# Kernel tuning notes

Measured on AMD Instinct MI355X. Metric: run time of the kernel, lower is better.

Reference implementation:

```python
import jax, jax.numpy as jnp
import numpy as np
from jax import lax

D_MODEL = 256
VOCAB = 512
D_INNER = 512          # expand=2
D_STATE = 64
D_CONV = 4
HEADDIM = 32
NHEADS = D_INNER // HEADDIM  # 16
NGROUPS = 1
CHUNK = 64
D_IN_PROJ = 2 * D_INNER + 2 * NGROUPS * D_STATE + NHEADS  # 1168
CONV_DIM = D_INNER + 2 * NGROUPS * D_STATE               # 640


def setup_inputs() -> dict:
    key = jax.random.key(0)
    ks = jax.random.split(key, 8)
    B, L = 8, 4096
    input_ids = jax.random.randint(ks[0], (B, L), 0, VOCAB)
    rn = lambda k, shp, sc: (jax.random.normal(k, shp) * sc).astype(jnp.float32)
    embed_w = rn(ks[1], (VOCAB, D_MODEL), 0.02).at[0].set(0.0)  # padding_idx=0
    in_proj_w = rn(ks[2], (D_IN_PROJ, D_MODEL), D_MODEL ** -0.5)
    conv_w = rn(ks[3], (CONV_DIM, D_CONV), 0.2)
    conv_b = jnp.zeros((CONV_DIM,), jnp.float32)
    A_log = jnp.log(jax.random.uniform(ks[4], (NHEADS,), minval=1.0, maxval=16.0)).astype(jnp.float32)
    D_skip = jnp.ones((NHEADS,), jnp.float32)
    dt0 = jax.random.uniform(ks[5], (NHEADS,), minval=1e-3, maxval=0.1)
    dt_bias = jnp.log(jnp.expm1(dt0)).astype(jnp.float32)  # inverse softplus
    gate_norm_w = jnp.ones((D_INNER,), jnp.float32)
    out_proj_w = rn(ks[6], (D_MODEL, D_INNER), D_INNER ** -0.5)
    norm_w = jnp.ones((D_MODEL,), jnp.float32)
    return dict(input_ids=input_ids, embed_w=embed_w, in_proj_w=in_proj_w,
                conv_w=conv_w, conv_b=conv_b, A_log=A_log, D_skip=D_skip,
                dt_bias=dt_bias, gate_norm_w=gate_norm_w, out_proj_w=out_proj_w,
                norm_w=norm_w)


def _rmsnorm(x, w, eps):
    return x * lax.rsqrt(jnp.mean(x * x, axis=-1, keepdims=True) + eps) * w


def _segsum(a):
    # a: (..., T) -> (..., T, T); out[q,s] = sum_{s+1..q} a, -inf above diag
    T = a.shape[-1]
    c = jnp.cumsum(a, axis=-1)
    seg = c[..., :, None] - c[..., None, :]
    mask = jnp.tril(jnp.ones((T, T), bool))
    return jnp.where(mask, seg, -jnp.inf)


def _ssd(X, A, Bm, Cm):
    # X:(b,l,h,p) already *dt ; A:(b,l,h)=dt*A_head ; Bm,Cm:(b,l,n)
    b, l, h, p = X.shape
    n = Bm.shape[-1]
    c, q = l // CHUNK, CHUNK
    X = X.reshape(b, c, q, h, p)
    A = A.reshape(b, c, q, h).transpose(0, 3, 1, 2)        # (b,h,c,q)
    Bm = Bm.reshape(b, c, q, n)
    Cm = Cm.reshape(b, c, q, n)
    A_cs = jnp.cumsum(A, axis=-1)                           # (b,h,c,q)
    Lmat = jnp.exp(_segsum(A))                              # (b,h,c,q,q)
    # intra-chunk (diagonal block) output
    Y_diag = jnp.einsum('bcqn,bckn,bhcqk,bckhp->bcqhp', Cm, Bm, Lmat, X)
    # states carried to end of each chunk
    decay_states = jnp.exp(A_cs[..., -1:] - A_cs)           # (b,h,c,q)
    states = jnp.einsum('bckn,bhck,bckhp->bchpn', Bm, decay_states, X)
    chunk_decay = jnp.exp(A_cs[..., -1])                    # (b,h,c)
    def step(hprev, inp):
        dec, st = inp
        return dec[..., None, None] * hprev + st, hprev
    _, prev = lax.scan(step, jnp.zeros((b, h, p, n), X.dtype),
                       (chunk_decay.transpose(2, 0, 1), states.transpose(1, 0, 2, 3, 4)))
    prev = prev.transpose(1, 0, 2, 3, 4)                    # (b,c,h,p,n)
    Y_off = jnp.einsum('bcqn,bchpn,bhcq->bcqhp', Cm, prev, jnp.exp(A_cs))
    return (Y_diag + Y_off).reshape(b, l, h, p)


def _mamba2(u, in_proj_w, conv_w, conv_b, A_log, D_skip, dt_bias, gate_norm_w, out_proj_w):
    B, L, _ = u.shape
    zxbcdt = u @ in_proj_w.T                                # (B,L,1168)
    z = zxbcdt[..., :D_INNER]
    xBC = zxbcdt[..., D_INNER:D_INNER + CONV_DIM]
    dt = zxbcdt[..., D_INNER + CONV_DIM:]                   # (B,L,H)
    # causal depthwise conv + silu
    xBC = lax.conv_general_dilated(xBC.transpose(0, 2, 1), conv_w[:, None, :],
                                   (1,), [(D_CONV - 1, 0)],
                                   dimension_numbers=('NCH', 'OIH', 'NCH'),
                                   feature_group_count=CONV_DIM)
    xBC = jax.nn.silu(xBC + conv_b[None, :, None]).transpose(0, 2, 1)
    x = xBC[..., :D_INNER].reshape(B, L, NHEADS, HEADDIM)
    Bm = xBC[..., D_INNER:D_INNER + D_STATE]
    Cm = xBC[..., D_INNER + D_STATE:]
    dt = jax.nn.softplus(dt + dt_bias)                      # (B,L,H)
    A = -jnp.exp(A_log)                                     # (H,)
    y = _ssd(x * dt[..., None], dt * A, Bm, Cm)
    y = y + D_skip[None, None, :, None] * x
    y = y.reshape(B, L, D_INNER)
    y = _rmsnorm(y * jax.nn.silu(z), gate_norm_w, 1e-5)     # RMSNormGated
    return y @ out_proj_w.T


def reference(input_ids, embed_w, in_proj_w, conv_w, conv_b, A_log, D_skip,
              dt_bias, gate_norm_w, out_proj_w, norm_w):
    x = embed_w[input_ids]                                  # (B,L,D)
    u = _rmsnorm(x, norm_w, 1e-6)
    x = x + _mamba2(u, in_proj_w, conv_w, conv_b, A_log, D_skip,
                    dt_bias, gate_norm_w, out_proj_w)
    logits = x @ embed_w.T                                  # tied lm_head
    return logits
```

## Files before the change

### kernel.cpp

```cpp
#include <hip/hip_runtime.h>
#include <cstdint>
#include <cstddef>

#define TOK    32768
#define BATCH  8
#define SEQ    4096
#define DMODEL 256
#define DINNER 512
#define DSTATE 64
#define NH     16
#define HD     32
#define DPROJ  1168
#define NPAD   1280
#define CONVD  640
#define VOCAB  512
#define HGRP   4
#define TS     132

typedef __attribute__((ext_vector_type(8))) short bf16x8;
typedef __attribute__((ext_vector_type(4))) float f32x4;

__device__ __forceinline__ unsigned short f2bf(float f) {
    unsigned u = __float_as_uint(f);
    u += 0x7fffu + ((u >> 16) & 1u);
    return (unsigned short)(u >> 16);
}
__device__ __forceinline__ float bf2f(short s) {
    return __uint_as_float(((unsigned)(unsigned short)s) << 16);
}
__device__ __forceinline__ unsigned cvtpk(float lo, float hi) {
    unsigned r;
    asm("v_cvt_pk_bf16_f32 %0, %1, %2" : "=v"(r) : "v"(lo), "v"(hi));
    return r;
}
__device__ __forceinline__ float fsilu(float s) {
    return s * __builtin_amdgcn_rcpf(1.f + __expf(-s));
}
__device__ __forceinline__ float sp(float v) {
    return v > 20.f ? v : __logf(1.f + __expf(v));
}

__device__ __forceinline__ void gload16(const short* src, short* dst) {
    __builtin_amdgcn_global_load_lds((const __attribute__((address_space(1))) void*)src,
                                     (__attribute__((address_space(3))) void*)dst, 16, 0, 0);
}

#define U16_OFF   0
#define Z16_OFF   (U16_OFF  + (size_t)TOK*128)
#define XBC_OFF   (Z16_OFF  + (size_t)TOK*256)
#define DTS_OFF   (XBC_OFF  + (size_t)TOK*320)
#define ACS_OFF   (DTS_OFF  + (size_t)TOK*16)
#define CDEC_OFF  (ACS_OFF  + (size_t)BATCH*NH*64*64)
#define WP_OFF    (CDEC_OFF + (size_t)BATCH*NH*64)
#define WO_OFF    (WP_OFF   + 163840)
#define WE_OFF    (WO_OFF   + 65536)
#define UNION_OFF (WE_OFF   + 65536)
#define UNION_FL  ((size_t)BATCH*64*NH*2048)
#define Y16_SUB   ((size_t)TOK*256)
#define WS_FLOATS (UNION_OFF + UNION_FL)

__global__ void k_diag(float* out, float wsmb) {
    if (blockIdx.x == 0 && threadIdx.x == 0) out[0] = wsmb;
}

__global__ void k_cvt(const float* __restrict__ s, short* __restrict__ d, int nsrc, int ntot) {
    int i = blockIdx.x * 256 + threadIdx.x;
    if (i < ntot) d[i] = (i < nsrc) ? (short)f2bf(s[i]) : (short)0;
}
__global__ void k_cvt_gate(const float* __restrict__ s, const float* __restrict__ gw,
                           short* __restrict__ d, int ntot) {
    int i = blockIdx.x * 256 + threadIdx.x;
    if (i < ntot) d[i] = (short)f2bf(s[i] * gw[i & (DINNER - 1)]);
}

__global__ void k_embed(const int* __restrict__ ids, const float* __restrict__ embed,
                        const float* __restrict__ norm_w, short* __restrict__ u16) {
    int t = blockIdx.x;
    int lane = threadIdx.x;
    int id = ids[t];
    float4 v = ((const float4*)(embed + (size_t)id * DMODEL))[lane];
    float ss = v.x*v.x + v.y*v.y + v.z*v.z + v.w*v.w;
    #pragma unroll
    for (int o = 32; o > 0; o >>= 1) ss += __shfl_down(ss, o);
    ss = __shfl(ss, 0);
    float r = rsqrtf(ss * (1.0f / DMODEL) + 1e-6f);
    float4 w = ((const float4*)norm_w)[lane];
    unsigned p0 = cvtpk(v.x * r * w.x, v.y * r * w.y);
    unsigned p1 = cvtpk(v.z * r * w.z, v.w * r * w.w);
    ((uint2*)(u16 + (size_t)t * DMODEL))[lane] = make_uint2(p0, p1);
}

template<int MODE>
__global__ __launch_bounds__(512) void k_gemm_mfma(
    const short* __restrict__ A, const short* __restrict__ B, int K,
    float* __restrict__ outF, short* __restrict__ z16, short* __restrict__ xbc,
    float* __restrict__ dts, const float* __restrict__ dt_bias,
    const float* __restrict__ cw, const float* __restrict__ cb) {
    __shared__ __align__(16) short SM[32768];
    constexpr int NX = (MODE == 0) ? (NPAD / 128) : (VOCAB / 128);
    int tid = threadIdx.x;
    int bid = blockIdx.x;
    int slot = bid >> 3;
    int m0 = (((bid & 7) * 32) + slot / NX) << 7;
    int n0 = (slot % NX) << 7;
    int wave = tid >> 6, lane = tid & 63;
    int wm = wave >> 1, wn = wave & 1;
    int lr = lane & 15, lg = lane >> 4;
    const f32x4 zer = {0.f, 0.f, 0.f, 0.f};
    f32x4 acc[2][4];
    #pragma unroll
    for (int i = 0; i < 2; i++)
        #pragma unroll
        for (int j = 0; j < 4; j++) acc[i][j] = zer;

    const bool isXBC = (MODE == 0) && (n0 >= 512) && (n0 < 1152);
    const bool atStart = (m0 & (SEQ - 1)) == 0;
    const bool haloLane = isXBC && (wm == 0) && !atStart && (lr < 3);
    f32x4 hacc[4];
    #pragma unroll
    for (int j = 0; j < 4; j++) hacc[j] = zer;
    const bf16x8 hz = {0, 0, 0, 0, 0, 0, 0, 0};
    bf16x8 hc0 = hz, hc1 = hz, hn0 = hz, hn1 = hz;

    const int nK = K >> 6;
    const int slo = lane >> 3;
    const int skb = ((lane & 7) ^ slo) << 3;

    {
        #pragma unroll
        for (int j = 0; j < 2; j++) {
            int row = wave * 16 + j * 8 + slo;
            gload16(A + (size_t)(m0 + row) * K + skb, SM + (wave * 2 + j) * 512);
            gload16(B + (size_t)(n0 + row) * K + skb, SM + 16384 + (wave * 2 + j) * 512);
        }
        if (haloLane) {
            hc0 = *(const bf16x8*)(A + (size_t)(m0 - 3 + lr) * K + lg * 8);
            hc1 = *(const bf16x8*)(A + (size_t)(m0 - 3 + lr) * K + 32 + lg * 8);
        }
    }
    __syncthreads();

    for (int kt = 0; kt < nK; ++kt) {
        if (kt + 1 < nK) {
            int k0 = (kt + 1) << 6;
            int nb = ((kt + 1) & 1) * 8192;
            #pragma unroll
            for (int j = 0; j < 2; j++) {
                int row = wave * 16 + j * 8 + slo;
                gload16(A + (size_t)(m0 + row) * K + k0 + skb, SM + nb + (wave * 2 + j) * 512);
                gload16(B + (size_t)(n0 + row) * K + k0 + skb, SM + 16384 + nb + (wave * 2 + j) * 512);
            }
            if (haloLane) {
                hn0 = *(const bf16x8*)(A + (size_t)(m0 - 3 + lr) * K + k0 + lg * 8);
                hn1 = *(const bf16x8*)(A + (size_t)(m0 - 3 + lr) * K + k0 + 32 + lg * 8);
            }
        }
        const short* CA = SM + (kt & 1) * 8192;
        const short* CB = SM + 16384 + (kt & 1) * 8192;
        #pragma unroll
        for (int kk = 0; kk < 2; kk++) {
            int sw = (((kk << 2) + lg) ^ (lr & 7)) << 3;
            bf16x8 af[2], bfr[4];
            #pragma unroll
            for (int mi = 0; mi < 2; mi++)
                af[mi] = *(const bf16x8*)&CA[(wm * 32 + mi * 16 + lr) * 64 + sw];
            #pragma unroll
            for (int ni = 0; ni < 4; ni++)
                bfr[ni] = *(const bf16x8*)&CB[(wn * 64 + ni * 16 + lr) * 64 + sw];
            #pragma unroll
            for (int mi = 0; mi < 2; mi++)
                #pragma unroll
                for (int ni = 0; ni < 4; ni++)
                    acc[mi][ni] = __builtin_amdgcn_mfma_f32_16x16x32_bf16(af[mi], bfr[ni], acc[mi][ni], 0, 0, 0);
            if (isXBC && wm == 0) {
                bf16x8 h = (kk == 0) ? hc0 : hc1;
                #pragma unroll
                for (int ni = 0; ni < 4; ni++)
                    hacc[ni] = __builtin_amdgcn_mfma_f32_16x16x32_bf16(h, bfr[ni], hacc[ni], 0, 0, 0);
            }
        }
        __syncthreads();
        hc0 = hn0; hc1 = hn1;
    }

    if (isXBC) {
        short* Tile = SM;
        #pragma unroll
        for (int mi = 0; mi < 2; mi++)
            #pragma unroll
            for (int ni = 0; ni < 4; ni++)
                #pragma unroll
                for (int r = 0; r < 4; r++) {
                    int row = wm * 32 + mi * 16 + lg * 4 + r;
                    int col = wn * 64 + ni * 16 + lr;
                    float v = acc[mi][ni][r];
                    float vo = __shfl_xor(v, 1);
                    if (!(lr & 1))
                        *(unsigned*)&Tile[(3 + row) * TS + col] = cvtpk(v, vo);
                }
        if (wm == 0 && lg == 0) {
            #pragma unroll
            for (int ni = 0; ni < 4; ni++)
                #pragma unroll
                for (int r = 0; r < 3; r++)
                    Tile[r * TS + wn * 64 + ni * 16 + lr] = (short)f2bf(hacc[ni][r]);
        }
        __syncthreads();
        int cp = tid & 63, rg = tid >> 6;
        int colb = cp * 2;
        int ch = (n0 - 512) + colb;
        float c0w0 = cw[ch * 4], c0w1 = cw[ch * 4 + 1], c0w2 = cw[ch * 4 + 2], c0w3 = cw[ch * 4 + 3];
        float c1w0 = cw[ch * 4 + 4], c1w1 = cw[ch * 4 + 5], c1w2 = cw[ch * 4 + 6], c1w3 = cw[ch * 4 + 7];
        float b0v = cb[ch], b1v = cb[ch + 1];
        int rbase = rg * 16;
        unsigned w0 = *(const unsigned*)&Tile[(rbase + 0) * TS + colb];
        unsigned w1 = *(const unsigned*)&Tile[(rbase + 1) * TS + colb];
        unsigned w2 = *(const unsigned*)&Tile[(rbase + 2) * TS + colb];
        for (int i = 0; i < 16; i++) {
            unsigned w3 = *(const unsigned*)&Tile[(rbase + i + 3) * TS + colb];
            float s0 = b0v, s1 = b1v;
            s0 = fmaf(bf2f((short)(w0 & 0xffffu)), c0w0, s0); s1 = fmaf(bf2f((short)(w0 >> 16)), c1w0, s1);
            s0 = fmaf(bf2f((short)(w1 & 0xffffu)), c0w1, s0); s1 = fmaf(bf2f((short)(w1 >> 16)), c1w1, s1);
            s0 = fmaf(bf2f((short)(w2 & 0xffffu)), c0w2, s0); s1 = fmaf(bf2f((short)(w2 >> 16)), c1w2, s1);
            s0 = fmaf(bf2f((short)(w3 & 0xffffu)), c0w3, s0); s1 = fmaf(bf2f((short)(w3 >> 16)), c1w3, s1);
            s0 = fsilu(s0);
            s1 = fsilu(s1);
            *(unsigned*)&xbc[(size_t)(m0 + rbase + i) * CONVD + ch] = cvtpk(s0, s1);
            w0 = w1; w1 = w2; w2 = w3;
        }
        return;
    }

    #pragma unroll
    for (int mi = 0; mi < 2; mi++) {
        #pragma unroll
        for (int r = 0; r < 4; r++) {
            int row = m0 + wm * 32 + mi * 16 + lg * 4 + r;
            #pragma unroll
            for (int ni = 0; ni < 4; ni++) {
                int col = n0 + wn * 64 + ni * 16 + lr;
                float v = acc[mi][ni][r];
                if (MODE == 0) {
                    if (n0 < 512) {
                        float vo = __shfl_xor(v, 1);
                        if (!(lr & 1))
                            *(unsigned*)&z16[(size_t)row * DINNER + col] = cvtpk(v, vo);
                    } else if (wn == 0 && ni == 0) {
                        dts[(size_t)row * NH + lr] = sp(v + dt_bias[lr]);
                    }
                } else {
                    outF[(size_t)row * VOCAB + col] = v;
                }
            }
        }
    }
}

__global__ __launch_bounds__(512) void k_outproj(
    const short* __restrict__ Y16, const short* __restrict__ z16,
    const short* __restrict__ Wo, const int* __restrict__ ids,
    const float* __restrict__ embed, short* __restrict__ xf16) {
    __shared__ __align__(16) short As[8192];
    __shared__ __align__(16) short Bs[8192];
    __shared__ float rmsS[128];
    int tid = threadIdx.x;
    int bid = blockIdx.x;
    int slot = bid >> 3;
    int m0 = (((bid & 7) * 32) + (slot >> 1)) << 7;
    int n0 = (slot & 1) << 7;
    int wave = tid >> 6, lane = tid & 63;
    int wm = wave >> 1, wn = wave & 1;
    int lr = lane & 15, lg = lane >> 4;
    const f32x4 zer = {0.f, 0.f, 0.f, 0.f};
    f32x4 acc[2][4];
    #pragma unroll
    for (int i = 0; i < 2; i++)
        #pragma unroll
        for (int j = 0; j < 4; j++) acc[i][j] = zer;

    const int arow = tid >> 2;
    const int ac0 = (tid & 3) * 2;
    const int slo = lane >> 3;
    const int skb = ((lane & 7) ^ slo) << 3;
    float ssq = 0.f;

    for (int kt = 0; kt < 8; ++kt) {
        int k0 = kt << 6;
        #pragma unroll
        for (int j = 0; j < 2; j++) {
            int row = wave * 16 + j * 8 + slo;
            gload16(Wo + (size_t)(n0 + row) * DINNER + k0 + skb, Bs + (wave * 2 + j) * 512);
        }
        union { int4 v; short s[8]; } y0u, y1u, z0u, z1u;
        const size_t rbase = (size_t)(m0 + arow) * DINNER + k0 + ac0 * 8;
        y0u.v = *(const int4*)(Y16 + rbase);
        y1u.v = *(const int4*)(Y16 + rbase + 8);
        z0u.v = *(const int4*)(z16 + rbase);
        z1u.v = *(const int4*)(z16 + rbase + 8);
        unsigned pk[8];
        #pragma unroll
        for (int e = 0; e < 4; e++) {
            float g0 = bf2f(y0u.s[2*e])     * fsilu(bf2f(z0u.s[2*e]));
            float g1 = bf2f(y0u.s[2*e + 1]) * fsilu(bf2f(z0u.s[2*e + 1]));
            ssq += g0 * g0 + g1 * g1;
            pk[e] = cvtpk(g0, g1);
        }
        #pragma unroll
        for (int e = 0; e < 4; e++) {
            float g0 = bf2f(y1u.s[2*e])     * fsilu(bf2f(z1u.s[2*e]));
            float g1 = bf2f(y1u.s[2*e + 1]) * fsilu(bf2f(z1u.s[2*e + 1]));
            ssq += g0 * g0 + g1 * g1;
            pk[4 + e] = cvtpk(g0, g1);
        }
        *(int4*)&As[arow * 64 + ((ac0 ^ (arow & 7)) << 3)] = *(int4*)&pk[0];
        *(int4*)&As[arow * 64 + (((ac0 + 1) ^ (arow & 7)) << 3)] = *(int4*)&pk[4];
        __syncthreads();
        #pragma unroll
        for (int kk = 0; kk < 2; kk++) {
            int sw = (((kk << 2) + lg) ^ (lr & 7)) << 3;
            bf16x8 af[2], bfr[4];
            #pragma unroll
            for (int mi = 0; mi < 2; mi++)
                af[mi] = *(const bf16x8*)&As[(wm * 32 + mi * 16 + lr) * 64 + sw];
            #pragma unroll
            for (int ni = 0; ni < 4; ni++)
                bfr[ni] = *(const bf16x8*)&Bs[(wn * 64 + ni * 16 + lr) * 64 + sw];
            #pragma unroll
            for (int mi = 0; mi < 2; mi++)
                #pragma unroll
                for (int ni = 0; ni < 4; ni++)
                    acc[mi][ni] = __builtin_amdgcn_mfma_f32_16x16x32_bf16(af[mi], bfr[ni], acc[mi][ni], 0, 0, 0);
        }
        __syncthreads();
    }
    ssq += __shfl_xor(ssq, 1);
    ssq += __shfl_xor(ssq, 2);
    if ((tid & 3) == 0) rmsS[arow] = rsqrtf(ssq * (1.0f / DINNER) + 1e-5f);
    __syncthreads();

    #pragma unroll
    for (int mi = 0; mi < 2; mi++) {
        #pragma unroll
        for (int r = 0; r < 4; r++) {
            int rl = wm * 32 + mi * 16 + lg * 4 + r;
            int row = m0 + rl;
            int id = ids[row];
            float rm = rmsS[rl];
            #pragma unroll
            for (int ni = 0; ni < 4; ni++) {
                int col = n0 + wn * 64 + ni * 16 + lr;
                float v = acc[mi][ni][r] * rm;
                float vo = __shfl_xor(v, 1);
                if (!(lr & 1)) {
                    float2 res = *(const float2*)&embed[(size_t)id * DMODEL + col];
                    *(unsigned*)&xf16[(size_t)row * DMODEL + col] = cvtpk(v + res.x, vo + res.y);
                }
            }
        }
    }
}

__global__ __launch_bounds__(256) void k_states(const short* __restrict__ xbc, const float* __restrict__ dts,
                                                const float* __restrict__ A_log,
                                                short* __restrict__ st16,
                                                float* __restrict__ acs_g, float* __restrict__ cdec) {
    __shared__ short BsB[64 * 72];
    __shared__ short BT[64 * 72];
    __shared__ short XdS[32 * 72];
    __shared__ __align__(16) short XKP[64 * 32];
    __shared__ float dkS[HGRP][64];
    __shared__ float dtS[64];
    int tid = threadIdx.x;
    int bid = blockIdx.x;
    int hg = bid & 3;
    int bc = bid >> 2;
    int b = bc >> 6, c = bc & 63;
    int h0 = hg * HGRP;
    size_t tbase = (size_t)b * SEQ + (size_t)c * 64;
    int wave = tid >> 6, lane = tid & 63;
    int lr = lane & 15, lg = lane >> 4;

    for (int i = tid; i < 64 * 64; i += 256) {
        int q = i >> 6, n = i & 63;
        BsB[q * 72 + n] = xbc[(tbase + q) * CONVD + DINNER + n];
    }
    {
        int h = h0 + wave;
        float Ah = -__expf(A_log[h]);
        float v = dts[(tbase + lane) * NH + h] * Ah;
        #pragma unroll
        for (int off = 1; off < 64; off <<= 1) {
            float o = __shfl_up(v, off);
            if (lane >= off) v += o;
        }
        acs_g[(((size_t)(b * NH + h)) * 64 + c) * 64 + lane] = v;
        float alast = __shfl(v, 63);
        dkS[wave][lane] = __expf(alast - v);
        if (lane == 0) cdec[(b * NH + h) * 64 + c] = __expf(alast);
    }
    __syncthreads();
    for (int i = tid; i < 64 * 64; i += 256) {
        int k = i >> 6, n = i & 63;
        BT[n * 72 + k] = BsB[k * 72 + n];
    }

    for (int hh = 0; hh < HGRP; hh++) {
        int h = h0 + hh;
        {
            int s = wave * 64 + lane;
            gload16(xbc + (tbase + (s >> 2)) * CONVD + h * HD + (s & 3) * 8, XKP + wave * 512);
        }
        if (tid < 64) dtS[tid] = dts[(tbase + tid) * NH + h];
        __syncthreads();
        for (int i = tid; i < 2048; i += 256) {
            int p = i & 31, k = i >> 5;
            XdS[p * 72 + k] = (short)f2bf(bf2f(XKP[k * 32 + p]) * dtS[k] * dkS[hh][k]);
        }
        __syncthreads();
        {
            int ptile = wave & 1;
            bf16x8 a0 = *(const bf16x8*)&XdS[(ptile * 16 + lr) * 72 + lg * 8];
            bf16x8 a1 = *(const bf16x8*)&XdS[(ptile * 16 + lr) * 72 + 32 + lg * 8];
            size_t base = ((size_t)bc * NH + h) * 2048;
            #pragma unroll
            for (int j = 0; j < 2; j++) {
                int nt = (wave >> 1) * 2 + j;
                bf16x8 b0 = *(const bf16x8*)&BT[(nt * 16 + lr) * 72 + lg * 8];
                bf16x8 b1 = *(const bf16x8*)&BT[(nt * 16 + lr) * 72 + 32 + lg * 8];
                f32x4 z = {0.f, 0.f, 0.f, 0.f};
                z = __builtin_amdgcn_mfma_f32_16x16x32_bf16(a0, b0, z, 0, 0, 0);
                z = __builtin_amdgcn_mfma_f32_16x16x32_bf16(a1, b1, z, 0, 0, 0);
                #pragma unroll
                for (int r = 0; r < 4; r++) {
                    int p = ptile * 16 + lg * 4 + r;
                    float v = z[r];
                    float vo = __shfl_xor(v, 1);
                    if (!(lr & 1)) {
                        int chunk = (nt << 1) | (lr >> 3);
                        *(unsigned*)&st16[base + p * 64 + ((chunk ^ (p & 7)) << 3) + (lr & 7)] = cvtpk(v, vo);
                    }
                }
            }
        }
        __syncthreads();
    }
}

__global__ __launch_bounds__(256) void k_scan(unsigned* __restrict__ st32, const float* __restrict__ cdec) {
    int bid = blockIdx.x;
    int bh = bid >> 2, seg = bid & 3;
    int b = bh >> 4, h = bh & 15;
    int off = seg * 256 + threadIdx.x;
    float p0 = 0.f, p1 = 0.f;
    for (int c = 0; c < 64; c++) {
        float dec = cdec[bh * 64 + c];
        size_t idx = ((((size_t)b * 64 + c) * NH) + h) * 1024 + off;
        unsigned v = st32[idx];
        float s0 = bf2f((short)(v & 0xffffu));
        float s1 = bf2f((short)(v >> 16));
        st32[idx] = cvtpk(p0, p1);
        p0 = fmaf(dec, p0, s0);
        p1 = fmaf(dec, p1, s1);
    }
}

__global__ __launch_bounds__(256) void k_y(const short* __restrict__ xbc, const float* __restrict__ dts,
                                           const short* __restrict__ st16, const float* __restrict__ acs_g,
                                           const float* __restrict__ D_skip, short* __restrict__ Y16) {
    __shared__ short CsB[64 * 72];
    __shared__ short Wsh[64 * 72];
    __shared__ short XtS[32 * 72];
    __shared__ __align__(16) short PtL[32 * 64];
    __shared__ __align__(16) short XKP[64 * 32];
    __shared__ float acsH[64];
    __shared__ float dtS[64];
    int tid = threadIdx.x;
    int bid = blockIdx.x;
    int hg = bid & 3;
    int bc = bid >> 2;
    int b = bc >> 6, c = bc & 63;
    int h0 = hg * HGRP;
    size_t tbase = (size_t)b * SEQ + (size_t)c * 64;
    int wave = tid >> 6, lane = tid & 63;
    int lr = lane & 15, lg = lane >> 4;

    for (int i = tid; i < 64 * 64; i += 256) {
        int q = i >> 6, n = i & 63;
        const short* rowp = xbc + (tbase + q) * CONVD + DINNER;
        Wsh[q * 72 + n] = rowp[n];
        CsB[q * 72 + n] = rowp[DSTATE + n];
    }
    __syncthreads();

    f32x4 macc[4];
    bf16x8 ca0 = *(const bf16x8*)&CsB[(wave * 16 + lr) * 72 + lg * 8];
    bf16x8 ca1 = *(const bf16x8*)&CsB[(wave * 16 + lr) * 72 + 32 + lg * 8];
    {
        #pragma unroll
        for (int ct = 0; ct < 4; ct++) {
            bf16x8 b0 = *(const bf16x8*)&Wsh[(ct * 16 + lr) * 72 + lg * 8];
            bf16x8 b1 = *(const bf16x8*)&Wsh[(ct * 16 + lr) * 72 + 32 + lg * 8];
            f32x4 z = {0.f, 0.f, 0.f, 0.f};
            z = __builtin_amdgcn_mfma_f32_16x16x32_bf16(ca0, b0, z, 0, 0, 0);
            z = __builtin_amdgcn_mfma_f32_16x16x32_bf16(ca1, b1, z, 0, 0, 0);
            macc[ct] = z;
        }
    }
    __syncthreads();

    for (int hh = 0; hh < HGRP; hh++) {
        int h = h0 + hh;
        {
            int s = wave * 64 + lane;
            gload16(xbc + (tbase + (s >> 2)) * CONVD + h * HD + (s & 3) * 8, XKP + wave * 512);
            gload16(st16 + ((size_t)bc * NH + h) * 2048 + s * 8, PtL + wave * 512);
        }
        if (tid < 64) {
            acsH[tid] = acs_g[(((size_t)(b * NH + h)) * 64 + c) * 64 + tid];
            dtS[tid] = dts[(tbase + tid) * NH + h];
        }
        __syncthreads();
        #pragma unroll
        for (int ct = 0; ct < 4; ct++) {
            int k = ct * 16 + lr;
            #pragma unroll
            for (int r = 0; r < 4; r++) {
                int q = wave * 16 + lg * 4 + r;
                float wv = 0.f;
                if (k <= q) wv = macc[ct][r] * __expf(acsH[q] - acsH[k]);
                float wo = __shfl_xor(wv, 1);
                if (!(lr & 1))
                    *(unsigned*)&Wsh[q * 72 + k] = cvtpk(wv, wo);
            }
        }
        for (int i = tid; i < 2048; i += 256) {
            int p = i & 31, k = i >> 5;
            XtS[p * 72 + k] = (short)f2bf(bf2f(XKP[k * 32 + p]) * dtS[k]);
        }
        __syncthreads();
        float eq[4];
        #pragma unroll
        for (int r = 0; r < 4; r++) eq[r] = __expf(acsH[wave * 16 + lg * 4 + r]);
        float dsk = D_skip[h];
        bf16x8 wa0 = *(const bf16x8*)&Wsh[(wave * 16 + lr) * 72 + lg * 8];
        bf16x8 wa1 = *(const bf16x8*)&Wsh[(wave * 16 + lr) * 72 + 32 + lg * 8];
        #pragma unroll
        for (int pt = 0; pt < 2; pt++) {
            int p = pt * 16 + lr;
            bf16x8 xb0 = *(const bf16x8*)&XtS[p * 72 + lg * 8];
            bf16x8 xb1 = *(const bf16x8*)&XtS[p * 72 + 32 + lg * 8];
            f32x4 zd = {0.f, 0.f, 0.f, 0.f};
            zd = __builtin_amdgcn_mfma_f32_16x16x32_bf16(wa0, xb0, zd, 0, 0, 0);
            zd = __builtin_amdgcn_mfma_f32_16x16x32_bf16(wa1, xb1, zd, 0, 0, 0);
            bf16x8 pb0 = *(const bf16x8*)&PtL[p * 64 + ((lg ^ (p & 7)) << 3)];
            bf16x8 pb1 = *(const bf16x8*)&PtL[p * 64 + (((lg + 4) ^ (p & 7)) << 3)];
            f32x4 zo = {0.f, 0.f, 0.f, 0.f};
            zo = __builtin_amdgcn_mfma_f32_16x16x32_bf16(ca0, pb0, zo, 0, 0, 0);
            zo = __builtin_amdgcn_mfma_f32_16x16x32_bf16(ca1, pb1, zo, 0, 0, 0);
            #pragma unroll
            for (int r = 0; r < 4; r++) {
                int q = wave * 16 + lg * 4 + r;
                float xv = bf2f(XKP[q * 32 + p]);
                float v = zd[r] + eq[r] * zo[r] + dsk * xv;
                float vo = __shfl_xor(v, 1);
                if (!(lr & 1))
                    *(unsigned*)&Y16[((tbase + q) * NH + h) * HD + p] = cvtpk(v, vo);
            }
        }
        __syncthreads();
    }
}

extern "C" void kernel_launch(void* const* d_in, const int* in_sizes, int n_in,
                              void* d_out, int out_size, void* d_ws, size_t ws_size,
                              hipStream_t stream) {
    const int*   ids        = (const int*)d_in[0];
    const float* embed_w    = (const float*)d_in[1];
    const float* in_proj_w  = (const float*)d_in[2];
    const float* conv_w     = (const float*)d_in[3];
    const float* conv_b     = (const float*)d_in[4];
    const float* A_log      = (const float*)d_in[5];
    const float* D_skip     = (const float*)d_in[6];
    const float* dt_bias    = (const float*)d_in[7];
    const float* gate_w     = (const float*)d_in[8];
    const float* out_proj_w = (const float*)d_in[9];
    const float* norm_w     = (const float*)d_in[10];
    float* out = (float*)d_out;

    if (ws_size < WS_FLOATS * sizeof(float)) {
        k_diag<<<1, 64, 0, stream>>>(out, (float)(ws_size >> 20));
        return;
    }

    float* ws   = (float*)d_ws;
    short* u16  = (short*)(ws + U16_OFF);
    short* z16  = (short*)(ws + Z16_OFF);
    short* xbc  = (short*)(ws + XBC_OFF);
    float* dts  = ws + DTS_OFF;
    float* acs  = ws + ACS_OFF;
    float* cdec = ws + CDEC_OFF;
    short* Wp   = (short*)(ws + WP_OFF);
    short* Wo   = (short*)(ws + WO_OFF);
    short* We   = (short*)(ws + WE_OFF);
    short* st16 = (short*)(ws + UNION_OFF);
    short* Y16  = (short*)(ws + UNION_OFF + Y16_SUB);
    short* xf16 = (short*)(ws + UNION_OFF);

    k_cvt<<<(NPAD * DMODEL + 255) / 256, 256, 0, stream>>>(in_proj_w, Wp, DPROJ * DMODEL, NPAD * DMODEL);
    k_cvt_gate<<<(DMODEL * DINNER + 255) / 256, 256, 0, stream>>>(out_proj_w, gate_w, Wo, DMODEL * DINNER);
    k_cvt<<<(VOCAB * DMODEL + 255) / 256, 256, 0, stream>>>(embed_w, We, VOCAB * DMODEL, VOCAB * DMODEL);
    k_embed<<<TOK, 64, 0, stream>>>(ids, embed_w, norm_w, u16);
    k_gemm_mfma<0><<<(NPAD / 128) * 256, 512, 0, stream>>>(
        u16, Wp, DMODEL, nullptr, z16, xbc, dts, dt_bias, conv_w, conv_b);
    k_states<<<BATCH * 64 * 4, 256, 0, stream>>>(xbc, dts, A_log, st16, acs, cdec);
    k_scan<<<BATCH * NH * 4, 256, 0, stream>>>((unsigned*)st16, cdec);
    k_y<<<BATCH * 64 * 4, 256, 0, stream>>>(xbc, dts, st16, acs, D_skip, Y16);
    k_outproj<<<(DMODEL / 128) * 256, 512, 0, stream>>>(Y16, z16, Wo, ids, embed_w, xf16);
    k_gemm_mfma<2><<<(VOCAB / 128) * 256, 512, 0, stream>>>(
        xf16, We, DMODEL, out, nullptr, nullptr, nullptr, nullptr, nullptr, nullptr);
}
```

Before: 220.4 us.

## Deepen GEMM prefetch to two stages with explicit vmcnt waits

```diff
diff --git a/kernel.cpp b/kernel.cpp
--- a/kernel.cpp
+++ b/kernel.cpp
@@ -116,45 +116,49 @@
     const bool isXBC = (MODE == 0) && (n0 >= 512) && (n0 < 1152);
     const bool atStart = (m0 & (SEQ - 1)) == 0;
     const bool haloLane = isXBC && (wm == 0) && !atStart && (lr < 3);
+    const bool haloWave = isXBC && (wm == 0) && !atStart;
     f32x4 hacc[4];
     #pragma unroll
     for (int j = 0; j < 4; j++) hacc[j] = zer;
     const bf16x8 hz = {0, 0, 0, 0, 0, 0, 0, 0};
-    bf16x8 hc0 = hz, hc1 = hz, hn0 = hz, hn1 = hz;
+    bf16x8 hA0 = hz, hA1 = hz;
+    bf16x8 hB0 = hz, hB1 = hz;
 
     const int nK = K >> 6;
     const int slo = lane >> 3;
     const int skb = ((lane & 7) ^ slo) << 3;
 
-    {
+    auto stage = [&](int kt2) {
+        int k0 = kt2 << 6;
+        int bsel = (kt2 & 1) * 8192;
         #pragma unroll
         for (int j = 0; j < 2; j++) {
             int row = wave * 16 + j * 8 + slo;
-            gload16(A + (size_t)(m0 + row) * K + skb, SM + (wave * 2 + j) * 512);
-            gload16(B + (size_t)(n0 + row) * K + skb, SM + 16384 + (wave * 2 + j) * 512);
-        }
-        if (haloLane) {
-            hc0 = *(const bf16x8*)(A + (size_t)(m0 - 3 + lr) * K + lg * 8);
-            hc1 = *(const bf16x8*)(A + (size_t)(m0 - 3 + lr) * K + 32 + lg * 8);
-        }
-    }
-    __syncthreads();
-
-    for (int kt = 0; kt < nK; ++kt) {
+            gload16(A + (size_t)(m0 + row) * K + k0 + skb, SM + bsel + (wave * 2 + j) * 512);
+            gload16(B + (size_t)(n0 + row) * K + k0 + skb, SM + 16384 + bsel + (wave * 2 + j) * 512);
+        }
+    };
+
+    stage(0);
+    if (haloLane) {
+        hA0 = *(const bf16x8*)(A + (size_t)(m0 - 3 + lr) * K + lg * 8);
+        hA1 = *(const bf16x8*)(A + (size_t)(m0 - 3 + lr) * K + 32 + lg * 8);
+    }
+    stage(1);
+    if (haloLane) {
+        hB0 = *(const bf16x8*)(A + (size_t)(m0 - 3 + lr) * K + 64 + lg * 8);
+        hB1 = *(const bf16x8*)(A + (size_t)(m0 - 3 + lr) * K + 96 + lg * 8);
+    }
+
+    auto body = [&](int kt, bf16x8& h0, bf16x8& h1) {
         if (kt + 1 < nK) {
-            int k0 = (kt + 1) << 6;
-            int nb = ((kt + 1) & 1) * 8192;
-            #pragma unroll
-            for (int j = 0; j < 2; j++) {
-                int row = wave * 16 + j * 8 + slo;
-                gload16(A + (size_t)(m0 + row) * K + k0 + skb, SM + nb + (wave * 2 + j) * 512);
-                gload16(B + (size_t)(n0 + row) * K + k0 + skb, SM + 16384 + nb + (wave * 2 + j) * 512);
-            }
-            if (haloLane) {
-                hn0 = *(const bf16x8*)(A + (size_t)(m0 - 3 + lr) * K + k0 + lg * 8);
-                hn1 = *(const bf16x8*)(A + (size_t)(m0 - 3 + lr) * K + k0 + 32 + lg * 8);
-            }
-        }
+            if (haloWave) asm volatile("s_waitcnt vmcnt(6)" ::: "memory");
+            else          asm volatile("s_waitcnt vmcnt(4)" ::: "memory");
+        } else {
+            asm volatile("s_waitcnt vmcnt(0)" ::: "memory");
+        }
+        __builtin_amdgcn_s_barrier();
+        __builtin_amdgcn_sched_barrier(0);
         const short* CA = SM + (kt & 1) * 8192;
         const short* CB = SM + 16384 + (kt & 1) * 8192;
         #pragma unroll
@@ -173,18 +177,33 @@
                 for (int ni = 0; ni < 4; ni++)
                     acc[mi][ni] = __builtin_amdgcn_mfma_f32_16x16x32_bf16(af[mi], bfr[ni], acc[mi][ni], 0, 0, 0);
             if (isXBC && wm == 0) {
-                bf16x8 h = (kk == 0) ? hc0 : hc1;
+                bf16x8 h = (kk == 0) ? h0 : h1;
                 #pragma unroll
                 for (int ni = 0; ni < 4; ni++)
                     hacc[ni] = __builtin_amdgcn_mfma_f32_16x16x32_bf16(h, bfr[ni], hacc[ni], 0, 0, 0);
             }
         }
-        __syncthreads();
-        hc0 = hn0; hc1 = hn1;
+        __builtin_amdgcn_sched_barrier(0);
+        __builtin_amdgcn_s_barrier();
+        __builtin_amdgcn_sched_barrier(0);
+        if (kt + 2 < nK) {
+            stage(kt + 2);
+            if (haloLane) {
+                int k0 = (kt + 2) << 6;
+                h0 = *(const bf16x8*)(A + (size_t)(m0 - 3 + lr) * K + k0 + lg * 8);
+                h1 = *(const bf16x8*)(A + (size_t)(m0 - 3 + lr) * K + k0 + 32 + lg * 8);
+            }
+        }
+    };
+
+    for (int kt = 0; kt < nK; kt += 2) {
+        body(kt, hA0, hA1);
+        body(kt + 1, hB0, hB1);
     }
 
     if (isXBC) {
         short* Tile = SM;
+        __syncthreads();
         #pragma unroll
         for (int mi = 0; mi < 2; mi++)
             #pragma unroll
```

Result: faster. 210.9 us (-4.3%).
